# Kernel optimization log

Hardware: AMD Instinct MI355X
Metric: run time of the kernel (lower is better)

The kernel has to match this reference:

```python
import jax, jax.numpy as jnp
import numpy as np

H = 64  # latent_dim // 2


def _lstm_cell(x, h, c, Wih, Whh, b):
    # PyTorch gate order: i, f, g, o
    g = x @ Wih.T + h @ Whh.T + b
    i, f, gg, o = jnp.split(g, 4, axis=-1)
    c = jax.nn.sigmoid(f) * c + jax.nn.sigmoid(i) * jnp.tanh(gg)
    h = jax.nn.sigmoid(o) * jnp.tanh(c)
    return h, c


def _run_lstm(x, Wih, Whh, b):
    # x: [B, T, D] -> outputs [B, T, H], final h, c (zero-initialized state)
    B = x.shape[0]
    h0 = jnp.zeros((B, Whh.shape[1]), x.dtype)

    def step(carry, xt):
        h, c = _lstm_cell(xt, carry[0], carry[1], Wih, Whh, b)
        return (h, c), h

    (h, c), ys = jax.lax.scan(step, (h0, h0), jnp.swapaxes(x, 0, 1))
    return jnp.swapaxes(ys, 0, 1), h, c


def setup_inputs() -> dict:
    key = jax.random.key(0)
    ks = jax.random.split(key, 16)
    B, S, T, D = 512, 1024, 512, 3
    s = 1.0 / np.sqrt(H)

    def u(k, shape):
        return jax.random.uniform(k, shape, jnp.float32, -s, s)

    return {
        "src": jax.random.normal(ks[0], (B, S, D), jnp.float32),
        "trg": jax.random.normal(ks[1], (B, T, D), jnp.float32),
        "enc1_Wih": u(ks[2], (4 * H, D)),
        "enc1_Whh": u(ks[3], (4 * H, H)),
        "enc1_b": u(ks[4], (4 * H,)),
        "enc2_Wih": u(ks[5], (4 * H, H)),
        "enc2_Whh": u(ks[6], (4 * H, H)),
        "enc2_b": u(ks[7], (4 * H,)),
        "dec1_Wih": u(ks[8], (4 * H, D)),
        "dec1_Whh": u(ks[9], (4 * H, H)),
        "dec1_b": u(ks[10], (4 * H,)),
        "dec2_Wih": u(ks[11], (4 * H, H)),
        "dec2_Whh": u(ks[12], (4 * H, H)),
        "dec2_b": u(ks[13], (4 * H,)),
        "fc_W": u(ks[14], (D, H)),
        "fc_b": u(ks[15], (D,)),
    }


def reference(src, trg, enc1_Wih, enc1_Whh, enc1_b, enc2_Wih, enc2_Whh, enc2_b,
              dec1_Wih, dec1_Whh, dec1_b, dec2_Wih, dec2_Whh, dec2_b, fc_W, fc_b):
    # Encoder: two stacked LSTMs over src; keep final state of layer 2.
    y1, _, _ = _run_lstm(src, enc1_Wih, enc1_Whh, enc1_b)
    _, h, c = _run_lstm(y1, enc2_Wih, enc2_Whh, enc2_b)

    # Decoder (teacher_forcing_ratio = 1.0, the only well-defined branch):
    # at each step both decoder LSTMs share/chain the SAME (h, c) state,
    # exactly as the original Decoder.forward does with seq-len-1 inputs.
    def step(carry, xt):
        h, c = carry
        h1, c1 = _lstm_cell(xt, h, c, dec1_Wih, dec1_Whh, dec1_b)
        h2, c2 = _lstm_cell(h1, h1, c1, dec2_Wih, dec2_Whh, dec2_b)
        return (h2, c2), h2 @ fc_W.T + fc_b

    xs = jnp.swapaxes(trg[:, :-1, :], 0, 1)  # inputs for t = 1..T-1
    _, preds = jax.lax.scan(step, (h, c), xs)
    preds = jnp.swapaxes(preds, 0, 1)  # [B, T-1, 3]

    B = trg.shape[0]
    zero0 = jnp.zeros((B, 1, fc_b.shape[0]), preds.dtype)  # outputs[:, 0] stays 0
    return jnp.concatenate([zero0, preds], axis=1)
```

## Files before the change

### kernel.cpp

```cpp
#include <hip/hip_runtime.h>
#include <math.h>

typedef _Float16 f16;
typedef _Float16 f16x8 __attribute__((ext_vector_type(8)));
typedef float    f32x4 __attribute__((ext_vector_type(4)));

#define MFMA16(A, B, C) __builtin_amdgcn_mfma_f32_16x16x32_f16((A), (B), (C), 0, 0, 0)
#define LOG2E 1.44269504088896f

__device__ __forceinline__ float sig2(float a) {
    return __builtin_amdgcn_rcpf(1.0f + __builtin_amdgcn_exp2f(a));
}
__device__ __forceinline__ float tanh2(float c) {
    return fmaf(2.0f, sig2(c * (-2.0f * LOG2E)), -1.0f);
}

__device__ __forceinline__ f16x8 ldfrag(const float* __restrict__ W, int n, int k0, float s) {
    const float* p = W + (size_t)n * 64 + k0;
    f16x8 r;
#pragma unroll
    for (int j = 0; j < 8; j++) r[j] = (f16)(s * p[j]);
    return r;
}

__global__ __launch_bounds__(512, 2)
void seq2seq_kernel(const float* __restrict__ src, const float* __restrict__ trg,
                    const float* __restrict__ e1ih, const float* __restrict__ e1hh,
                    const float* __restrict__ e1b,
                    const float* __restrict__ e2ih, const float* __restrict__ e2hh,
                    const float* __restrict__ e2b,
                    const float* __restrict__ d1ih, const float* __restrict__ d1hh,
                    const float* __restrict__ d1b,
                    const float* __restrict__ d2ih, const float* __restrict__ d2hh,
                    const float* __restrict__ d2b,
                    const float* __restrict__ fcW, const float* __restrict__ fcb,
                    float* __restrict__ out)
{
    const int bp   = blockIdx.x;
    const int tid  = threadIdx.x;
    const int wv   = tid >> 6;
    const bool isB = (wv >= 4);
    const int wvg  = wv & 3;
    const int lane = tid & 63;
    const int quad = lane >> 4;
    const int c15  = lane & 15;
    const int u16  = wvg * 16 + c15;
    const int qb   = quad & 1;
    const int ab   = c15 & 1;

    __shared__ __align__(16) float xst[1024][8];
    __shared__ __align__(16) float tst[512][8];
    __shared__ __align__(16) f16 h1l[2][2][64];
    __shared__ __align__(16) f16 h2l[2][2][64];
    __shared__ float c1buf[2][64];
    __shared__ float c2buf[2][64];
    __shared__ __align__(16) f16 ring[2][16][72];

    {
        const float* s0 = src + (size_t)(2 * bp) * 3072;
        const float* s1 = s0 + 3072;
        for (int i = tid; i < 3072; i += 512) {
            int t = i / 3, c = i - 3 * t;
            xst[t][c]     = s0[i];
            xst[t][4 + c] = s1[i];
        }
        const float* t0p = trg + (size_t)(2 * bp) * 1536;
        const float* t1p = t0p + 1536;
        for (int i = tid; i < 1536; i += 512) {
            int t = i / 3, c = i - 3 * t;
            tst[t][c]     = t0p[i];
            tst[t][4 + c] = t1p[i];
        }
    }

    f16x8 E1hh[4][2];
    f16x8 E2ih[4][2], E2hh[4][2];
    float xw[4][3], bias1[4];
    f32x4 bs2[4];
    if (!isB) {
#pragma unroll
        for (int g = 0; g < 4; g++) {
            const float s = (g == 2) ? (-2.0f * LOG2E) : (-LOG2E);
            const int n = g * 64 + u16;
#pragma unroll
            for (int c = 0; c < 2; c++)
                E1hh[g][c] = ldfrag(e1hh, n, c * 32 + quad * 8, s);
            xw[g][0] = s * e1ih[n * 3 + 0];
            xw[g][1] = s * e1ih[n * 3 + 1];
            xw[g][2] = s * e1ih[n * 3 + 2];
            bias1[g] = s * e1b[n];
        }
    } else {
#pragma unroll
        for (int g = 0; g < 4; g++) {
            const float s = (g == 2) ? (-2.0f * LOG2E) : (-LOG2E);
            const int n = g * 64 + u16;
#pragma unroll
            for (int c = 0; c < 2; c++) {
                E2ih[g][c] = ldfrag(e2ih, n, c * 32 + quad * 8, s);
                E2hh[g][c] = ldfrag(e2hh, n, c * 32 + quad * 8, s);
            }
            float bv = s * e2b[n];
            bs2[g] = (f32x4){bv, bv, bv, bv};
        }
    }

    float c1 = 0.f, c2 = 0.f;
    if (tid < 256) {
        (&h1l[0][0][0])[tid] = (f16)0.f;
        (&h2l[0][0][0])[tid] = (f16)0.f;
    }
    __syncthreads();

    const f32x4 z4 = {0.f, 0.f, 0.f, 0.f};

    f32x4 xq = z4, xnq = z4;
    if (!isB) xq = *(const f32x4*)&xst[0][qb * 4];

#pragma unroll 1
    for (int tau = 0; tau <= 1024; tau++) {
        const int w = tau & 1;
        if (!isB) {
            if (tau < 1024) {
                const f16* h1p = h1l[w ^ 1][ab];
                f16x8 a0 = *(const f16x8*)(h1p + quad * 8);
                f16x8 a1 = *(const f16x8*)(h1p + 32 + quad * 8);
                float xt[4];
#pragma unroll
                for (int g = 0; g < 4; g++)
                    xt[g] = fmaf(xw[g][0], xq.x,
                            fmaf(xw[g][1], xq.y, fmaf(xw[g][2], xq.z, bias1[g])));
                f32x4 acc[4];
#pragma unroll
                for (int g = 0; g < 4; g++)
                    acc[g] = MFMA16(a1, E1hh[g][1], MFMA16(a0, E1hh[g][0], z4));
                float v[4];
#pragma unroll
                for (int g = 0; g < 4; g++)
                    v[g] = (qb ? acc[g][1] : acc[g][0]) + xt[g];
                float iv = sig2(v[0]), fv = sig2(v[1]);
                float gv = fmaf(2.0f, sig2(v[2]), -1.0f), ov = sig2(v[3]);
                c1 = fv * c1 + iv * gv;
                if (quad < 2) h1l[w][quad][u16] = (f16)(ov * tanh2(c1));
                const int tn = (tau + 1 < 1024) ? tau + 1 : 1023;
                xnq = *(const f32x4*)&xst[tn][qb * 4];
            }
        } else {
            if (tau > 0) {
                const f16* h1p = h1l[w ^ 1][ab];
                const f16* h2p = h2l[w ^ 1][ab];
                f16x8 a0 = *(const f16x8*)(h1p + quad * 8);
                f16x8 a1 = *(const f16x8*)(h1p + 32 + quad * 8);
                f16x8 b0 = *(const f16x8*)(h2p + quad * 8);
                f16x8 b1 = *(const f16x8*)(h2p + 32 + quad * 8);
                f32x4 accA[4], accB[4];
#pragma unroll
                for (int g = 0; g < 4; g++) {
                    accA[g] = MFMA16(a1, E2ih[g][1], MFMA16(a0, E2ih[g][0], bs2[g]));
                    accB[g] = MFMA16(b1, E2hh[g][1], MFMA16(b0, E2hh[g][0], z4));
                }
                float v[4];
#pragma unroll
                for (int g = 0; g < 4; g++)
                    v[g] = (qb ? accA[g][1] : accA[g][0]) +
                           (qb ? accB[g][1] : accB[g][0]);
                float iv = sig2(v[0]), fv = sig2(v[1]);
                float gv = fmaf(2.0f, sig2(v[2]), -1.0f), ov = sig2(v[3]);
                c2 = fv * c2 + iv * gv;
                if (quad < 2) h2l[w][quad][u16] = (f16)(ov * tanh2(c2));
            }
        }
        __syncthreads();
        if (!isB) xq = xnq;
    }

    f16x8 D1hh[4][2];
    f16x8 W2s[4][2];
    float dxw[4][3], db1[4];
    f32x4 db2s[4];
    if (!isB) {
#pragma unroll
        for (int g = 0; g < 4; g++) {
            const float s = (g == 2) ? (-2.0f * LOG2E) : (-LOG2E);
            const int n = g * 64 + u16;
#pragma unroll
            for (int c = 0; c < 2; c++)
                D1hh[g][c] = ldfrag(d1hh, n, c * 32 + quad * 8, s);
            dxw[g][0] = s * d1ih[n * 3 + 0];
            dxw[g][1] = s * d1ih[n * 3 + 1];
            dxw[g][2] = s * d1ih[n * 3 + 2];
            db1[g] = s * d1b[n];
        }
    } else {
#pragma unroll
        for (int g = 0; g < 4; g++) {
            const float s = (g == 2) ? (-2.0f * LOG2E) : (-LOG2E);
            const int n = g * 64 + u16;
#pragma unroll
            for (int c = 0; c < 2; c++) {
                const int k0 = c * 32 + quad * 8;
                const float* pa = d2ih + (size_t)n * 64 + k0;
                const float* pb = d2hh + (size_t)n * 64 + k0;
                f16x8 r;
#pragma unroll
                for (int j = 0; j < 8; j++) r[j] = (f16)(s * (pa[j] + pb[j]));
                W2s[g][c] = r;
            }
            float bv = s * d2b[n];
            db2s[g] = (f32x4){bv, bv, bv, bv};
        }
        if (quad < 2) c2buf[quad][u16] = c2;
    }
    f16x8 FW0 = {}, FW1 = {};
    float fb = 0.f;
    if (wv >= 6 && c15 < 3) {
#pragma unroll
        for (int j = 0; j < 8; j++) {
            FW0[j] = (f16)fcW[c15 * 64 + quad * 8 + j];
            FW1[j] = (f16)fcW[c15 * 64 + 32 + quad * 8 + j];
        }
        fb = fcb[c15];
    }
    __syncthreads();

    f32x4 tq = z4, tnq = z4;
    if (!isB) tq = *(const f32x4*)&tst[0][qb * 4];

#pragma unroll 1
    for (int t = 0; t < 511; t++) {
        const int r = t & 1, w = r ^ 1;
        if (!isB) {
            const f16* hp = h2l[r][ab];
            f16x8 a0 = *(const f16x8*)(hp + quad * 8);
            f16x8 a1 = *(const f16x8*)(hp + 32 + quad * 8);
            float cdin = c2buf[qb][u16];
            float xt[4];
#pragma unroll
            for (int g = 0; g < 4; g++)
                xt[g] = fmaf(dxw[g][0], tq.x,
                        fmaf(dxw[g][1], tq.y, fmaf(dxw[g][2], tq.z, db1[g])));
            f32x4 acc[4];
#pragma unroll
            for (int g = 0; g < 4; g++)
                acc[g] = MFMA16(a1, D1hh[g][1], MFMA16(a0, D1hh[g][0], z4));
            float v[4];
#pragma unroll
            for (int g = 0; g < 4; g++)
                v[g] = (qb ? acc[g][1] : acc[g][0]) + xt[g];
            float iv = sig2(v[0]), fv = sig2(v[1]);
            float gv = fmaf(2.0f, sig2(v[2]), -1.0f), ov = sig2(v[3]);
            float c1d = fv * cdin + iv * gv;
            if (quad < 2) {
                h1l[w][quad][u16] = (f16)(ov * tanh2(c1d));
                c1buf[quad][u16]  = c1d;
            }
            const int tn = (t + 1 < 511) ? t + 1 : 510;
            tnq = *(const f32x4*)&tst[tn][qb * 4];
        } else if (wv >= 6 && t > 0 && (t & 15) == 0) {
            const int bsel = wv - 6;
            const f16* rp = &ring[bsel][0][0];
            f16x8 fa0 = *(const f16x8*)(rp + c15 * 72 + quad * 8);
            f16x8 fa1 = *(const f16x8*)(rp + c15 * 72 + 32 + quad * 8);
            f32x4 acc = MFMA16(fa1, FW1, MFMA16(fa0, FW0, z4));
            if (c15 < 3) {
                float* ob = out + (((size_t)(2 * bp + bsel) * 512 + (t - 15)) * 3) + c15;
#pragma unroll
                for (int rg = 0; rg < 4; rg++)
                    ob[(quad * 4 + rg) * 3] = acc[rg] + fb;
            }
        }
        __syncthreads();
        if (!isB) tq = tnq;

        if (isB) {
            const f16* np = h1l[w][ab];
            f16x8 m0 = *(const f16x8*)(np + quad * 8);
            f16x8 m1 = *(const f16x8*)(np + 32 + quad * 8);
            float c1in = c1buf[qb][u16];
            f32x4 acc[4];
#pragma unroll
            for (int g = 0; g < 4; g++)
                acc[g] = MFMA16(m1, W2s[g][1], MFMA16(m0, W2s[g][0], db2s[g]));
            float v[4];
#pragma unroll
            for (int g = 0; g < 4; g++)
                v[g] = (qb ? acc[g][1] : acc[g][0]);
            float i2 = sig2(v[0]), f2 = sig2(v[1]);
            float g2 = fmaf(2.0f, sig2(v[2]), -1.0f), o2 = sig2(v[3]);
            float c2d = f2 * c1in + i2 * g2;
            if (quad < 2) {
                f16 hh = (f16)(o2 * tanh2(c2d));
                h2l[w][quad][u16] = hh;
                c2buf[quad][u16]  = c2d;
                ring[quad][t & 15][u16] = hh;
            }
        }
        __syncthreads();
    }

    if (wv >= 6) {
        const int bsel = wv - 6;
        const f16* rp = &ring[bsel][0][0];
        f16x8 fa0 = *(const f16x8*)(rp + c15 * 72 + quad * 8);
        f16x8 fa1 = *(const f16x8*)(rp + c15 * 72 + 32 + quad * 8);
        f32x4 acc = MFMA16(fa1, FW1, MFMA16(fa0, FW0, z4));
        if (c15 < 3) {
            float* ob = out + (((size_t)(2 * bp + bsel) * 512 + 497) * 3) + c15;
#pragma unroll
            for (int rg = 0; rg < 4; rg++) {
                int step = quad * 4 + rg;
                if (step < 15) ob[step * 3] = acc[rg] + fb;
            }
        }
    }
}

extern "C" void kernel_launch(void* const* d_in, const int* in_sizes, int n_in,
                              void* d_out, int out_size, void* d_ws, size_t ws_size,
                              hipStream_t stream)
{
    const float* src   = (const float*)d_in[0];
    const float* trg   = (const float*)d_in[1];
    const float* e1ih  = (const float*)d_in[2];
    const float* e1hh  = (const float*)d_in[3];
    const float* e1b   = (const float*)d_in[4];
    const float* e2ih  = (const float*)d_in[5];
    const float* e2hh  = (const float*)d_in[6];
    const float* e2b   = (const float*)d_in[7];
    const float* dd1ih = (const float*)d_in[8];
    const float* dd1hh = (const float*)d_in[9];
    const float* dd1b  = (const float*)d_in[10];
    const float* dd2ih = (const float*)d_in[11];
    const float* dd2hh = (const float*)d_in[12];
    const float* dd2b  = (const float*)d_in[13];
    const float* fcW   = (const float*)d_in[14];
    const float* fcb   = (const float*)d_in[15];
    float* out = (float*)d_out;

    hipMemsetAsync(d_out, 0, (size_t)out_size * sizeof(float), stream);

    seq2seq_kernel<<<256, 512, 0, stream>>>(src, trg,
                                            e1ih, e1hh, e1b, e2ih, e2hh, e2b,
                                            dd1ih, dd1hh, dd1b, dd2ih, dd2hh, dd2b,
                                            fcW, fcb, out);
}
```

Measured before the change: 834.8 us.

## Split encoder layer-2 input projection into a third wave group pipeline stage

Expands the block from 8 to 12 waves and splits encoder layer 2 so one group computes the Wih·h1 projection one step ahead and writes it to LDS, while another group does the recurrent Whh part. This shortens the per-step critical path of the layer-2 wavefronts, giving a three-stage pipeline across the 1024 encoder steps. The cost is an extra pipeline step, more threads per block, and an LDS padding array that limits occupancy. Decoder roles are remapped so the new wave group stays idle there.

```diff
diff --git a/kernel.cpp b/kernel.cpp
--- a/kernel.cpp
+++ b/kernel.cpp
@@ -23,7 +23,7 @@
     return r;
 }
 
-__global__ __launch_bounds__(512, 2)
+__global__ __launch_bounds__(768, 3)
 void seq2seq_kernel(const float* __restrict__ src, const float* __restrict__ trg,
                     const float* __restrict__ e1ih, const float* __restrict__ e1hh,
                     const float* __restrict__ e1b,
@@ -39,7 +39,7 @@
     const int bp   = blockIdx.x;
     const int tid  = threadIdx.x;
     const int wv   = tid >> 6;
-    const bool isB = (wv >= 4);
+    const int grp  = wv >> 2;
     const int wvg  = wv & 3;
     const int lane = tid & 63;
     const int quad = lane >> 4;
@@ -52,21 +52,25 @@
     __shared__ __align__(16) float tst[512][8];
     __shared__ __align__(16) f16 h1l[2][2][64];
     __shared__ __align__(16) f16 h2l[2][2][64];
+    __shared__ __align__(16) float pihl[2][2][64][4];
     __shared__ float c1buf[2][64];
     __shared__ float c2buf[2][64];
     __shared__ __align__(16) f16 ring[2][16][72];
+    __shared__ float lds_pad[6400];
+
+    lds_pad[tid] = 0.f;
 
     {
         const float* s0 = src + (size_t)(2 * bp) * 3072;
         const float* s1 = s0 + 3072;
-        for (int i = tid; i < 3072; i += 512) {
+        for (int i = tid; i < 3072; i += 768) {
             int t = i / 3, c = i - 3 * t;
             xst[t][c]     = s0[i];
             xst[t][4 + c] = s1[i];
         }
         const float* t0p = trg + (size_t)(2 * bp) * 1536;
         const float* t1p = t0p + 1536;
-        for (int i = tid; i < 1536; i += 512) {
+        for (int i = tid; i < 1536; i += 768) {
             int t = i / 3, c = i - 3 * t;
             tst[t][c]     = t0p[i];
             tst[t][4 + c] = t1p[i];
@@ -74,10 +78,11 @@
     }
 
     f16x8 E1hh[4][2];
-    f16x8 E2ih[4][2], E2hh[4][2];
+    f16x8 E2hh[4][2];
+    f16x8 E2ih[4][2];
     float xw[4][3], bias1[4];
     f32x4 bs2[4];
-    if (!isB) {
+    if (grp == 0) {
 #pragma unroll
         for (int g = 0; g < 4; g++) {
             const float s = (g == 2) ? (-2.0f * LOG2E) : (-LOG2E);
@@ -90,18 +95,25 @@
             xw[g][2] = s * e1ih[n * 3 + 2];
             bias1[g] = s * e1b[n];
         }
-    } else {
-#pragma unroll
-        for (int g = 0; g < 4; g++) {
-            const float s = (g == 2) ? (-2.0f * LOG2E) : (-LOG2E);
-            const int n = g * 64 + u16;
-#pragma unroll
-            for (int c = 0; c < 2; c++) {
-                E2ih[g][c] = ldfrag(e2ih, n, c * 32 + quad * 8, s);
+    } else if (grp == 1) {
+#pragma unroll
+        for (int g = 0; g < 4; g++) {
+            const float s = (g == 2) ? (-2.0f * LOG2E) : (-LOG2E);
+            const int n = g * 64 + u16;
+#pragma unroll
+            for (int c = 0; c < 2; c++)
                 E2hh[g][c] = ldfrag(e2hh, n, c * 32 + quad * 8, s);
-            }
             float bv = s * e2b[n];
             bs2[g] = (f32x4){bv, bv, bv, bv};
+        }
+    } else {
+#pragma unroll
+        for (int g = 0; g < 4; g++) {
+            const float s = (g == 2) ? (-2.0f * LOG2E) : (-LOG2E);
+            const int n = g * 64 + u16;
+#pragma unroll
+            for (int c = 0; c < 2; c++)
+                E2ih[g][c] = ldfrag(e2ih, n, c * 32 + quad * 8, s);
         }
     }
 
@@ -115,14 +127,13 @@
     const f32x4 z4 = {0.f, 0.f, 0.f, 0.f};
 
     f32x4 xq = z4, xnq = z4;
-    if (!isB) xq = *(const f32x4*)&xst[0][qb * 4];
+    if (grp == 0) xq = *(const f32x4*)&xst[0][qb * 4];
 
 #pragma unroll 1
-    for (int tau = 0; tau <= 1024; tau++) {
-        const int w = tau & 1;
-        if (!isB) {
+    for (int tau = 0; tau <= 1025; tau++) {
+        if (grp == 0) {
             if (tau < 1024) {
-                const f16* h1p = h1l[w ^ 1][ab];
+                const f16* h1p = h1l[(tau + 1) & 1][ab];
                 f16x8 a0 = *(const f16x8*)(h1p + quad * 8);
                 f16x8 a1 = *(const f16x8*)(h1p + 32 + quad * 8);
                 float xt[4];
@@ -141,44 +152,55 @@
                 float iv = sig2(v[0]), fv = sig2(v[1]);
                 float gv = fmaf(2.0f, sig2(v[2]), -1.0f), ov = sig2(v[3]);
                 c1 = fv * c1 + iv * gv;
-                if (quad < 2) h1l[w][quad][u16] = (f16)(ov * tanh2(c1));
+                if (quad < 2) h1l[tau & 1][quad][u16] = (f16)(ov * tanh2(c1));
                 const int tn = (tau + 1 < 1024) ? tau + 1 : 1023;
                 xnq = *(const f32x4*)&xst[tn][qb * 4];
             }
-        } else {
-            if (tau > 0) {
-                const f16* h1p = h1l[w ^ 1][ab];
-                const f16* h2p = h2l[w ^ 1][ab];
+        } else if (grp == 2) {
+            if (tau >= 1 && tau <= 1024) {
+                const f16* h1p = h1l[(tau + 1) & 1][ab];
                 f16x8 a0 = *(const f16x8*)(h1p + quad * 8);
                 f16x8 a1 = *(const f16x8*)(h1p + 32 + quad * 8);
+                f32x4 acc[4];
+#pragma unroll
+                for (int g = 0; g < 4; g++)
+                    acc[g] = MFMA16(a1, E2ih[g][1], MFMA16(a0, E2ih[g][0], z4));
+                if (quad < 2) {
+                    f32x4 pv;
+#pragma unroll
+                    for (int g = 0; g < 4; g++) pv[g] = acc[g][quad];
+                    *(f32x4*)&pihl[(tau + 1) & 1][quad][u16][0] = pv;
+                }
+            }
+        } else {
+            if (tau >= 2) {
+                const f16* h2p = h2l[(tau + 1) & 1][ab];
                 f16x8 b0 = *(const f16x8*)(h2p + quad * 8);
                 f16x8 b1 = *(const f16x8*)(h2p + 32 + quad * 8);
-                f32x4 accA[4], accB[4];
-#pragma unroll
-                for (int g = 0; g < 4; g++) {
-                    accA[g] = MFMA16(a1, E2ih[g][1], MFMA16(a0, E2ih[g][0], bs2[g]));
-                    accB[g] = MFMA16(b1, E2hh[g][1], MFMA16(b0, E2hh[g][0], z4));
-                }
+                f32x4 pv = *(const f32x4*)&pihl[tau & 1][qb][u16][0];
+                f32x4 acc[4];
+#pragma unroll
+                for (int g = 0; g < 4; g++)
+                    acc[g] = MFMA16(b1, E2hh[g][1], MFMA16(b0, E2hh[g][0], bs2[g]));
                 float v[4];
 #pragma unroll
                 for (int g = 0; g < 4; g++)
-                    v[g] = (qb ? accA[g][1] : accA[g][0]) +
-                           (qb ? accB[g][1] : accB[g][0]);
+                    v[g] = (qb ? acc[g][1] : acc[g][0]) + pv[g];
                 float iv = sig2(v[0]), fv = sig2(v[1]);
                 float gv = fmaf(2.0f, sig2(v[2]), -1.0f), ov = sig2(v[3]);
                 c2 = fv * c2 + iv * gv;
-                if (quad < 2) h2l[w][quad][u16] = (f16)(ov * tanh2(c2));
+                if (quad < 2) h2l[tau & 1][quad][u16] = (f16)(ov * tanh2(c2));
             }
         }
         __syncthreads();
-        if (!isB) xq = xnq;
+        if (grp == 0) xq = xnq;
     }
 
     f16x8 D1hh[4][2];
     f16x8 W2s[4][2];
     float dxw[4][3], db1[4];
     f32x4 db2s[4];
-    if (!isB) {
+    if (grp == 0) {
 #pragma unroll
         for (int g = 0; g < 4; g++) {
             const float s = (g == 2) ? (-2.0f * LOG2E) : (-LOG2E);
@@ -191,7 +213,7 @@
             dxw[g][2] = s * d1ih[n * 3 + 2];
             db1[g] = s * d1b[n];
         }
-    } else {
+    } else if (grp == 1) {
 #pragma unroll
         for (int g = 0; g < 4; g++) {
             const float s = (g == 2) ? (-2.0f * LOG2E) : (-LOG2E);
@@ -213,7 +235,7 @@
     }
     f16x8 FW0 = {}, FW1 = {};
     float fb = 0.f;
-    if (wv >= 6 && c15 < 3) {
+    if ((wv == 8 || wv == 9) && c15 < 3) {
 #pragma unroll
         for (int j = 0; j < 8; j++) {
             FW0[j] = (f16)fcW[c15 * 64 + quad * 8 + j];
@@ -224,12 +246,12 @@
     __syncthreads();
 
     f32x4 tq = z4, tnq = z4;
-    if (!isB) tq = *(const f32x4*)&tst[0][qb * 4];
+    if (grp == 0) tq = *(const f32x4*)&tst[0][qb * 4];
 
 #pragma unroll 1
     for (int t = 0; t < 511; t++) {
-        const int r = t & 1, w = r ^ 1;
-        if (!isB) {
+        const int w = t & 1, r = w ^ 1;
+        if (grp == 0) {
             const f16* hp = h2l[r][ab];
             f16x8 a0 = *(const f16x8*)(hp + quad * 8);
             f16x8 a1 = *(const f16x8*)(hp + 32 + quad * 8);
@@ -256,8 +278,8 @@
             }
             const int tn = (t + 1 < 511) ? t + 1 : 510;
             tnq = *(const f32x4*)&tst[tn][qb * 4];
-        } else if (wv >= 6 && t > 0 && (t & 15) == 0) {
-            const int bsel = wv - 6;
+        } else if ((wv == 8 || wv == 9) && t > 0 && (t & 15) == 0) {
+            const int bsel = wv - 8;
             const f16* rp = &ring[bsel][0][0];
             f16x8 fa0 = *(const f16x8*)(rp + c15 * 72 + quad * 8);
             f16x8 fa1 = *(const f16x8*)(rp + c15 * 72 + 32 + quad * 8);
@@ -270,9 +292,9 @@
             }
         }
         __syncthreads();
-        if (!isB) tq = tnq;
-
-        if (isB) {
+        if (grp == 0) tq = tnq;
+
+        if (grp == 1) {
             const f16* np = h1l[w][ab];
             f16x8 m0 = *(const f16x8*)(np + quad * 8);
             f16x8 m1 = *(const f16x8*)(np + 32 + quad * 8);
@@ -298,8 +320,8 @@
         __syncthreads();
     }
 
-    if (wv >= 6) {
-        const int bsel = wv - 6;
+    if (wv == 8 || wv == 9) {
+        const int bsel = wv - 8;
         const f16* rp = &ring[bsel][0][0];
         f16x8 fa0 = *(const f16x8*)(rp + c15 * 72 + quad * 8);
         f16x8 fa1 = *(const f16x8*)(rp + c15 * 72 + 32 + quad * 8);
@@ -339,7 +361,7 @@
 
     hipMemsetAsync(d_out, 0, (size_t)out_size * sizeof(float), stream);
 
-    seq2seq_kernel<<<256, 512, 0, stream>>>(src, trg,
+    seq2seq_kernel<<<256, 768, 0, stream>>>(src, trg,
                                             e1ih, e1hh, e1b, e2ih, e2hh, e2b,
                                             dd1ih, dd1hh, dd1b, dd2ih, dd2hh, dd2b,
                                             fcW, fcb, out);
```

Result: slower. 851.6 us (+2.0%).

## Pipeline decoder layers across two batch rows and split gate activations across lanes

Applied to the files above, without the earlier changes.

The decoder loop no longer runs layer 1 then layer 2 for both batch rows with two barriers per step. It interleaves the two rows as a software pipeline: wave group A runs dec1 for one row while group B runs dec2 for the other, using one barrier per half-step over 1023 phases. A new cell_act helper gives the i/f gates to the lower lane quads and the g/o gates to the upper ones, swapping results with a lane shuffle, so each lane computes two sigmoids instead of four. This trades fewer barriers and less transcendental work for extra shuffles and more complicated ring and output indexing, where off-by-one mistakes are a risk.

```diff
diff --git a/kernel.cpp b/kernel.cpp
--- a/kernel.cpp
+++ b/kernel.cpp
@@ -13,6 +13,21 @@
 }
 __device__ __forceinline__ float tanh2(float c) {
     return fmaf(2.0f, sig2(c * (-2.0f * LOG2E)), -1.0f);
+}
+__device__ __forceinline__ float xor32(float v) {
+    return __shfl_xor(v, 32, 64);
+}
+
+__device__ __forceinline__ float cell_act(const float v[4], float& c, int quad) {
+    float va = (quad < 2) ? v[0] : v[2];
+    float vb = (quad < 2) ? v[1] : v[3];
+    float sa = sig2(va);
+    float sb = sig2(vb);
+    sa = (quad < 2) ? sa : fmaf(2.0f, sa, -1.0f);
+    float xa = xor32(sa);
+    float xb = xor32(sb);
+    c = fmaf(sb, c, sa * xa);
+    return xb * tanh2(c);
 }
 
 __device__ __forceinline__ f16x8 ldfrag(const float* __restrict__ W, int n, int k0, float s) {
@@ -52,6 +67,8 @@
     __shared__ __align__(16) float tst[512][8];
     __shared__ __align__(16) f16 h1l[2][2][64];
     __shared__ __align__(16) f16 h2l[2][2][64];
+    __shared__ __align__(16) f16 hDl[2][64];
+    __shared__ __align__(16) f16 h1dl[2][64];
     __shared__ float c1buf[2][64];
     __shared__ float c2buf[2][64];
     __shared__ __align__(16) f16 ring[2][16][72];
@@ -106,6 +123,7 @@
     }
 
     float c1 = 0.f, c2 = 0.f;
+    float h2last = 0.f;
     if (tid < 256) {
         (&h1l[0][0][0])[tid] = (f16)0.f;
         (&h2l[0][0][0])[tid] = (f16)0.f;
@@ -138,10 +156,8 @@
 #pragma unroll
                 for (int g = 0; g < 4; g++)
                     v[g] = (qb ? acc[g][1] : acc[g][0]) + xt[g];
-                float iv = sig2(v[0]), fv = sig2(v[1]);
-                float gv = fmaf(2.0f, sig2(v[2]), -1.0f), ov = sig2(v[3]);
-                c1 = fv * c1 + iv * gv;
-                if (quad < 2) h1l[w][quad][u16] = (f16)(ov * tanh2(c1));
+                float h1n = cell_act(v, c1, quad);
+                if (quad < 2) h1l[w][quad][u16] = (f16)h1n;
                 const int tn = (tau + 1 < 1024) ? tau + 1 : 1023;
                 xnq = *(const f32x4*)&xst[tn][qb * 4];
             }
@@ -164,10 +180,9 @@
                 for (int g = 0; g < 4; g++)
                     v[g] = (qb ? accA[g][1] : accA[g][0]) +
                            (qb ? accB[g][1] : accB[g][0]);
-                float iv = sig2(v[0]), fv = sig2(v[1]);
-                float gv = fmaf(2.0f, sig2(v[2]), -1.0f), ov = sig2(v[3]);
-                c2 = fv * c2 + iv * gv;
-                if (quad < 2) h2l[w][quad][u16] = (f16)(ov * tanh2(c2));
+                float h2n = cell_act(v, c2, quad);
+                h2last = h2n;
+                if (quad < 2) h2l[w][quad][u16] = (f16)h2n;
             }
         }
         __syncthreads();
@@ -209,7 +224,10 @@
             float bv = s * d2b[n];
             db2s[g] = (f32x4){bv, bv, bv, bv};
         }
-        if (quad < 2) c2buf[quad][u16] = c2;
+        if (quad < 2) {
+            hDl[quad][u16]  = (f16)h2last;
+            c2buf[quad][u16] = c2;
+        }
     }
     f16x8 FW0 = {}, FW1 = {};
     float fb = 0.f;
@@ -224,78 +242,93 @@
     __syncthreads();
 
     f32x4 tq = z4, tnq = z4;
-    if (!isB) tq = *(const f32x4*)&tst[0][qb * 4];
+    if (!isB) tq = *(const f32x4*)&tst[0][0];
 
 #pragma unroll 1
-    for (int t = 0; t < 511; t++) {
-        const int r = t & 1, w = r ^ 1;
+    for (int p = 0; p < 1023; p++) {
+        const int b = p & 1;
         if (!isB) {
-            const f16* hp = h2l[r][ab];
-            f16x8 a0 = *(const f16x8*)(hp + quad * 8);
-            f16x8 a1 = *(const f16x8*)(hp + 32 + quad * 8);
-            float cdin = c2buf[qb][u16];
-            float xt[4];
-#pragma unroll
-            for (int g = 0; g < 4; g++)
-                xt[g] = fmaf(dxw[g][0], tq.x,
-                        fmaf(dxw[g][1], tq.y, fmaf(dxw[g][2], tq.z, db1[g])));
-            f32x4 acc[4];
-#pragma unroll
-            for (int g = 0; g < 4; g++)
-                acc[g] = MFMA16(a1, D1hh[g][1], MFMA16(a0, D1hh[g][0], z4));
-            float v[4];
-#pragma unroll
-            for (int g = 0; g < 4; g++)
-                v[g] = (qb ? acc[g][1] : acc[g][0]) + xt[g];
-            float iv = sig2(v[0]), fv = sig2(v[1]);
-            float gv = fmaf(2.0f, sig2(v[2]), -1.0f), ov = sig2(v[3]);
-            float c1d = fv * cdin + iv * gv;
-            if (quad < 2) {
-                h1l[w][quad][u16] = (f16)(ov * tanh2(c1d));
-                c1buf[quad][u16]  = c1d;
-            }
-            const int tn = (t + 1 < 511) ? t + 1 : 510;
-            tnq = *(const f32x4*)&tst[tn][qb * 4];
-        } else if (wv >= 6 && t > 0 && (t & 15) == 0) {
-            const int bsel = wv - 6;
-            const f16* rp = &ring[bsel][0][0];
-            f16x8 fa0 = *(const f16x8*)(rp + c15 * 72 + quad * 8);
-            f16x8 fa1 = *(const f16x8*)(rp + c15 * 72 + 32 + quad * 8);
-            f32x4 acc = MFMA16(fa1, FW1, MFMA16(fa0, FW0, z4));
-            if (c15 < 3) {
-                float* ob = out + (((size_t)(2 * bp + bsel) * 512 + (t - 15)) * 3) + c15;
-#pragma unroll
-                for (int rg = 0; rg < 4; rg++)
-                    ob[(quad * 4 + rg) * 3] = acc[rg] + fb;
+            if (p < 1022) {
+                const f16* hp = hDl[b];
+                f16x8 a0 = *(const f16x8*)(hp + quad * 8);
+                f16x8 a1 = *(const f16x8*)(hp + 32 + quad * 8);
+                float cdin = c2buf[b][u16];
+                float xt[4];
+#pragma unroll
+                for (int g = 0; g < 4; g++)
+                    xt[g] = fmaf(dxw[g][0], tq.x,
+                            fmaf(dxw[g][1], tq.y, fmaf(dxw[g][2], tq.z, db1[g])));
+                f32x4 acc[4];
+#pragma unroll
+                for (int g = 0; g < 4; g++)
+                    acc[g] = MFMA16(a1, D1hh[g][1], MFMA16(a0, D1hh[g][0], z4));
+                float v[4];
+#pragma unroll
+                for (int g = 0; g < 4; g++)
+                    v[g] = acc[g][0] + xt[g];
+                float cc = cdin;
+                float h1d = cell_act(v, cc, quad);
+                if (quad == 0) {
+                    h1dl[b][u16]  = (f16)h1d;
+                    c1buf[b][u16] = cc;
+                }
+                const int pn = (p + 1 < 1022) ? p + 1 : p;
+                tnq = *(const f32x4*)&tst[pn >> 1][(pn & 1) * 4];
+            }
+        } else {
+            if (p > 0) {
+                const int bb = 1 - b;
+                const int tb = (p - 1) >> 1;
+                const f16* np = h1dl[bb];
+                f16x8 m0 = *(const f16x8*)(np + quad * 8);
+                f16x8 m1 = *(const f16x8*)(np + 32 + quad * 8);
+                float c1in = c1buf[bb][u16];
+                f32x4 acc[4];
+#pragma unroll
+                for (int g = 0; g < 4; g++)
+                    acc[g] = MFMA16(m1, W2s[g][1], MFMA16(m0, W2s[g][0], db2s[g]));
+                float v[4];
+#pragma unroll
+                for (int g = 0; g < 4; g++)
+                    v[g] = acc[g][0];
+                float cc = c1in;
+                float hh = cell_act(v, cc, quad);
+                if (quad == 0) {
+                    f16 hf = (f16)hh;
+                    hDl[bb][u16]  = hf;
+                    c2buf[bb][u16] = cc;
+                    ring[bb][tb & 15][u16] = hf;
+                }
+            }
+            if (wv == 6 && (p & 31) == 0 && p >= 32 && p <= 992) {
+                const int t = p >> 1;
+                const f16* rp = &ring[0][0][0];
+                f16x8 fa0 = *(const f16x8*)(rp + c15 * 72 + quad * 8);
+                f16x8 fa1 = *(const f16x8*)(rp + c15 * 72 + 32 + quad * 8);
+                f32x4 facc = MFMA16(fa1, FW1, MFMA16(fa0, FW0, z4));
+                if (c15 < 3) {
+                    float* ob = out + (((size_t)(2 * bp) * 512 + (t - 15)) * 3) + c15;
+#pragma unroll
+                    for (int rg = 0; rg < 4; rg++)
+                        ob[(quad * 4 + rg) * 3] = facc[rg] + fb;
+                }
+            }
+            if (wv == 7 && (p & 31) == 1 && p >= 33 && p <= 993) {
+                const int t = p >> 1;
+                const f16* rp = &ring[1][0][0];
+                f16x8 fa0 = *(const f16x8*)(rp + c15 * 72 + quad * 8);
+                f16x8 fa1 = *(const f16x8*)(rp + c15 * 72 + 32 + quad * 8);
+                f32x4 facc = MFMA16(fa1, FW1, MFMA16(fa0, FW0, z4));
+                if (c15 < 3) {
+                    float* ob = out + (((size_t)(2 * bp + 1) * 512 + (t - 15)) * 3) + c15;
+#pragma unroll
+                    for (int rg = 0; rg < 4; rg++)
+                        ob[(quad * 4 + rg) * 3] = facc[rg] + fb;
+                }
             }
         }
         __syncthreads();
         if (!isB) tq = tnq;
-
-        if (isB) {
-            const f16* np = h1l[w][ab];
-            f16x8 m0 = *(const f16x8*)(np + quad * 8);
-            f16x8 m1 = *(const f16x8*)(np + 32 + quad * 8);
-            float c1in = c1buf[qb][u16];
-            f32x4 acc[4];
-#pragma unroll
-            for (int g = 0; g < 4; g++)
-                acc[g] = MFMA16(m1, W2s[g][1], MFMA16(m0, W2s[g][0], db2s[g]));
-            float v[4];
-#pragma unroll
-            for (int g = 0; g < 4; g++)
-                v[g] = (qb ? acc[g][1] : acc[g][0]);
-            float i2 = sig2(v[0]), f2 = sig2(v[1]);
-            float g2 = fmaf(2.0f, sig2(v[2]), -1.0f), o2 = sig2(v[3]);
-            float c2d = f2 * c1in + i2 * g2;
-            if (quad < 2) {
-                f16 hh = (f16)(o2 * tanh2(c2d));
-                h2l[w][quad][u16] = hh;
-                c2buf[quad][u16]  = c2d;
-                ring[quad][t & 15][u16] = hh;
-            }
-        }
-        __syncthreads();
     }
 
     if (wv >= 6) {
@@ -303,13 +336,13 @@
         const f16* rp = &ring[bsel][0][0];
         f16x8 fa0 = *(const f16x8*)(rp + c15 * 72 + quad * 8);
         f16x8 fa1 = *(const f16x8*)(rp + c15 * 72 + 32 + quad * 8);
-        f32x4 acc = MFMA16(fa1, FW1, MFMA16(fa0, FW0, z4));
+        f32x4 facc = MFMA16(fa1, FW1, MFMA16(fa0, FW0, z4));
         if (c15 < 3) {
             float* ob = out + (((size_t)(2 * bp + bsel) * 512 + 497) * 3) + c15;
 #pragma unroll
             for (int rg = 0; rg < 4; rg++) {
                 int step = quad * 4 + rg;
-                if (step < 15) ob[step * 3] = acc[rg] + fb;
+                if (step < 15) ob[step * 3] = facc[rg] + fb;
             }
         }
     }
```

Result: slower. 1.055 ms (+26.3%).

## Run decoder cells redundantly in both wave groups, keep cell state in registers

Applied to the files above, without the earlier changes.

Both wave groups now compute both decoder LSTM cells each step. Waves 0-3 publish h1 and h2 to shared memory, and waves 4-7 write h2 only to the output ring. The c1/c2 cell states stay in registers, so the c1buf/c2buf shared-memory round trips go away. The idle half of each phase no longer sits waiting, and cell state no longer has to be shared. The price is double the MFMA and transcendental work, plus each wave holding both decoder weight sets in registers, which raises register pressure.

```diff
diff --git a/kernel.cpp b/kernel.cpp
--- a/kernel.cpp
+++ b/kernel.cpp
@@ -52,8 +52,7 @@
     __shared__ __align__(16) float tst[512][8];
     __shared__ __align__(16) f16 h1l[2][2][64];
     __shared__ __align__(16) f16 h2l[2][2][64];
-    __shared__ float c1buf[2][64];
-    __shared__ float c2buf[2][64];
+    __shared__ float c2seed[2][64];
     __shared__ __align__(16) f16 ring[2][16][72];
 
     {
@@ -174,43 +173,32 @@
         if (!isB) xq = xnq;
     }
 
-    f16x8 D1hh[4][2];
-    f16x8 W2s[4][2];
+    f16x8 D1hh[4][2], W2s[4][2];
     float dxw[4][3], db1[4];
     f32x4 db2s[4];
-    if (!isB) {
-#pragma unroll
-        for (int g = 0; g < 4; g++) {
-            const float s = (g == 2) ? (-2.0f * LOG2E) : (-LOG2E);
-            const int n = g * 64 + u16;
-#pragma unroll
-            for (int c = 0; c < 2; c++)
-                D1hh[g][c] = ldfrag(d1hh, n, c * 32 + quad * 8, s);
-            dxw[g][0] = s * d1ih[n * 3 + 0];
-            dxw[g][1] = s * d1ih[n * 3 + 1];
-            dxw[g][2] = s * d1ih[n * 3 + 2];
-            db1[g] = s * d1b[n];
-        }
-    } else {
-#pragma unroll
-        for (int g = 0; g < 4; g++) {
-            const float s = (g == 2) ? (-2.0f * LOG2E) : (-LOG2E);
-            const int n = g * 64 + u16;
-#pragma unroll
-            for (int c = 0; c < 2; c++) {
-                const int k0 = c * 32 + quad * 8;
-                const float* pa = d2ih + (size_t)n * 64 + k0;
-                const float* pb = d2hh + (size_t)n * 64 + k0;
-                f16x8 r;
-#pragma unroll
-                for (int j = 0; j < 8; j++) r[j] = (f16)(s * (pa[j] + pb[j]));
-                W2s[g][c] = r;
-            }
-            float bv = s * d2b[n];
-            db2s[g] = (f32x4){bv, bv, bv, bv};
-        }
-        if (quad < 2) c2buf[quad][u16] = c2;
-    }
+#pragma unroll
+    for (int g = 0; g < 4; g++) {
+        const float s = (g == 2) ? (-2.0f * LOG2E) : (-LOG2E);
+        const int n = g * 64 + u16;
+#pragma unroll
+        for (int c = 0; c < 2; c++) {
+            const int k0 = c * 32 + quad * 8;
+            D1hh[g][c] = ldfrag(d1hh, n, k0, s);
+            const float* pa = d2ih + (size_t)n * 64 + k0;
+            const float* pb = d2hh + (size_t)n * 64 + k0;
+            f16x8 r;
+#pragma unroll
+            for (int j = 0; j < 8; j++) r[j] = (f16)(s * (pa[j] + pb[j]));
+            W2s[g][c] = r;
+        }
+        dxw[g][0] = s * d1ih[n * 3 + 0];
+        dxw[g][1] = s * d1ih[n * 3 + 1];
+        dxw[g][2] = s * d1ih[n * 3 + 2];
+        db1[g] = s * d1b[n];
+        float bv = s * d2b[n];
+        db2s[g] = (f32x4){bv, bv, bv, bv};
+    }
+    if (isB && quad < 2) c2seed[quad][u16] = c2;
     f16x8 FW0 = {}, FW1 = {};
     float fb = 0.f;
     if (wv >= 6 && c15 < 3) {
@@ -223,17 +211,18 @@
     }
     __syncthreads();
 
-    f32x4 tq = z4, tnq = z4;
-    if (!isB) tq = *(const f32x4*)&tst[0][qb * 4];
+    float c2r = c2seed[qb][u16];
+    float c1r = 0.f;
+
+    f32x4 tq = *(const f32x4*)&tst[0][qb * 4], tnq = z4;
 
 #pragma unroll 1
     for (int t = 0; t < 511; t++) {
         const int r = t & 1, w = r ^ 1;
-        if (!isB) {
+        {
             const f16* hp = h2l[r][ab];
             f16x8 a0 = *(const f16x8*)(hp + quad * 8);
             f16x8 a1 = *(const f16x8*)(hp + 32 + quad * 8);
-            float cdin = c2buf[qb][u16];
             float xt[4];
 #pragma unroll
             for (int g = 0; g < 4; g++)
@@ -249,34 +238,30 @@
                 v[g] = (qb ? acc[g][1] : acc[g][0]) + xt[g];
             float iv = sig2(v[0]), fv = sig2(v[1]);
             float gv = fmaf(2.0f, sig2(v[2]), -1.0f), ov = sig2(v[3]);
-            float c1d = fv * cdin + iv * gv;
-            if (quad < 2) {
-                h1l[w][quad][u16] = (f16)(ov * tanh2(c1d));
-                c1buf[quad][u16]  = c1d;
-            }
+            c1r = fv * c2r + iv * gv;
+            if (wv < 4 && quad < 2) h1l[w][quad][u16] = (f16)(ov * tanh2(c1r));
             const int tn = (t + 1 < 511) ? t + 1 : 510;
             tnq = *(const f32x4*)&tst[tn][qb * 4];
-        } else if (wv >= 6 && t > 0 && (t & 15) == 0) {
+        }
+        if (wv >= 6 && t > 0 && (t & 15) == 0) {
             const int bsel = wv - 6;
             const f16* rp = &ring[bsel][0][0];
             f16x8 fa0 = *(const f16x8*)(rp + c15 * 72 + quad * 8);
             f16x8 fa1 = *(const f16x8*)(rp + c15 * 72 + 32 + quad * 8);
-            f32x4 acc = MFMA16(fa1, FW1, MFMA16(fa0, FW0, z4));
+            f32x4 facc = MFMA16(fa1, FW1, MFMA16(fa0, FW0, z4));
             if (c15 < 3) {
                 float* ob = out + (((size_t)(2 * bp + bsel) * 512 + (t - 15)) * 3) + c15;
 #pragma unroll
                 for (int rg = 0; rg < 4; rg++)
-                    ob[(quad * 4 + rg) * 3] = acc[rg] + fb;
+                    ob[(quad * 4 + rg) * 3] = facc[rg] + fb;
             }
         }
         __syncthreads();
-        if (!isB) tq = tnq;
-
-        if (isB) {
+
+        {
             const f16* np = h1l[w][ab];
             f16x8 m0 = *(const f16x8*)(np + quad * 8);
             f16x8 m1 = *(const f16x8*)(np + 32 + quad * 8);
-            float c1in = c1buf[qb][u16];
             f32x4 acc[4];
 #pragma unroll
             for (int g = 0; g < 4; g++)
@@ -287,15 +272,16 @@
                 v[g] = (qb ? acc[g][1] : acc[g][0]);
             float i2 = sig2(v[0]), f2 = sig2(v[1]);
             float g2 = fmaf(2.0f, sig2(v[2]), -1.0f), o2 = sig2(v[3]);
-            float c2d = f2 * c1in + i2 * g2;
+            c2r = f2 * c1r + i2 * g2;
+            float hh = o2 * tanh2(c2r);
             if (quad < 2) {
-                f16 hh = (f16)(o2 * tanh2(c2d));
-                h2l[w][quad][u16] = hh;
-                c2buf[quad][u16]  = c2d;
-                ring[quad][t & 15][u16] = hh;
+                f16 hf = (f16)hh;
+                if (wv < 4) h2l[w][quad][u16] = hf;
+                else        ring[quad][t & 15][u16] = hf;
             }
         }
         __syncthreads();
+        tq = tnq;
     }
 
     if (wv >= 6) {
@@ -303,13 +289,13 @@
         const f16* rp = &ring[bsel][0][0];
         f16x8 fa0 = *(const f16x8*)(rp + c15 * 72 + quad * 8);
         f16x8 fa1 = *(const f16x8*)(rp + c15 * 72 + 32 + quad * 8);
-        f32x4 acc = MFMA16(fa1, FW1, MFMA16(fa0, FW0, z4));
+        f32x4 facc = MFMA16(fa1, FW1, MFMA16(fa0, FW0, z4));
         if (c15 < 3) {
             float* ob = out + (((size_t)(2 * bp + bsel) * 512 + 497) * 3) + c15;
 #pragma unroll
             for (int rg = 0; rg < 4; rg++) {
                 int step = quad * 4 + rg;
-                if (step < 15) ob[step * 3] = acc[rg] + fb;
+                if (step < 15) ob[step * 3] = facc[rg] + fb;
             }
         }
     }
```

Result: slower. 931.0 us (+11.5%).
